# Optimization experiments

Hardware: AMD Instinct MI355X
Metric: run time of the kernel (lower is better)

## Reference

```python
import jax, jax.numpy as jnp
import numpy as np

B, T, C = 4, 2048, 1024
N_HEAD = 16
HEAD_DIM = C // N_HEAD


def setup_inputs() -> dict:
    key = jax.random.key(0)
    k1, k2, k3, k4, k5 = jax.random.split(key, 5)
    s = 0.02
    return {
        "x": jax.random.normal(k1, (B, T, C), dtype=jnp.float32),
        "w_attn": jax.random.normal(k2, (C, 3 * C), dtype=jnp.float32) * s,
        "b_attn": jnp.zeros((3 * C,), dtype=jnp.float32),
        "w_proj": jax.random.normal(k3, (C, C), dtype=jnp.float32) * s,
        "b_proj": jnp.zeros((C,), dtype=jnp.float32),
    }


def reference(x, w_attn, b_attn, w_proj, b_proj):
    Bb, Tt, Cc = x.shape
    qkv = x @ w_attn + b_attn                      # [B,T,3C]
    q, k, v = jnp.split(qkv, 3, axis=-1)
    # [B,T,C] -> [B,H,T,D]
    def heads(t):
        return t.reshape(Bb, Tt, N_HEAD, HEAD_DIM).transpose(0, 2, 1, 3)
    q, k, v = heads(q), heads(k), heads(v)
    scale = 1.0 / (HEAD_DIM ** 0.5)
    att = jnp.einsum('bhqd,bhkd->bhqk', q, k) * scale
    causal = jnp.tril(jnp.ones((Tt, Tt), dtype=bool))
    att = jnp.where(causal, att, -jnp.inf)
    att = jax.nn.softmax(att, axis=-1)             # dropout p=0.0 -> identity
    y = jnp.einsum('bhqk,bhkd->bhqd', att, v)
    y = y.transpose(0, 2, 1, 3).reshape(Bb, Tt, Cc)
    return y @ w_proj + b_proj
```

## Files before the change

kernel.cpp:

```cpp
#include <hip/hip_runtime.h>
#include <hip/hip_bf16.h>

typedef unsigned short u16;
typedef unsigned int u32;
typedef __bf16 bf16_t;
typedef bf16_t bf16x8 __attribute__((ext_vector_type(8)));
typedef float f32x4 __attribute__((ext_vector_type(4)));
typedef u16 u16x4 __attribute__((ext_vector_type(4)));
typedef u32 u32x2 __attribute__((ext_vector_type(2)));
typedef u32 u32x4 __attribute__((ext_vector_type(4)));
typedef int intx2 __attribute__((ext_vector_type(2)));

#define MFMA16(a, b, c) __builtin_amdgcn_mfma_f32_16x16x32_bf16((a), (b), (c), 0, 0, 0)

#define QSCL 0.18033688011112042f

__device__ __forceinline__ u16 f2b(float f) {
  bf16_t h = (bf16_t)f;
  return __builtin_bit_cast(u16, h);
}

__device__ __forceinline__ void gload_lds16(const void* src, void* dst) {
  __builtin_amdgcn_global_load_lds(
      (const __attribute__((address_space(1))) void*)src,
      (__attribute__((address_space(3))) void*)dst, 16, 0, 0);
}

__device__ __forceinline__ bf16x8 frag_read(const u16* tile, int row, int kchunk) {
  int off = row * 128 + ((kchunk ^ (row & 7)) << 4);
  return *reinterpret_cast<const bf16x8*>(reinterpret_cast<const char*>(tile) + off);
}

__device__ __forceinline__ void stage128(const u16* g, int rowStrideElts, u16* tile, int tid) {
  int lane = tid & 63, w = tid >> 6;
#pragma unroll
  for (int i = 0; i < 4; ++i) {
    int r = w * 32 + i * 8 + (lane >> 3);
    int cs = (lane & 7) ^ (r & 7);
    gload_lds16(g + (size_t)r * rowStrideElts + cs * 8, tile + r * 64 + (lane & 7) * 8);
  }
}

__global__ __launch_bounds__(256) void cvt_f32_bf16(const float* __restrict__ in,
                                                    u16* __restrict__ out, int n4) {
  int i = blockIdx.x * 256 + threadIdx.x;
  if (i < n4) {
    float4 f = reinterpret_cast<const float4*>(in)[i];
    ushort4 o;
    o.x = f2b(f.x); o.y = f2b(f.y); o.z = f2b(f.z); o.w = f2b(f.w);
    reinterpret_cast<ushort4*>(out)[i] = o;
  }
}

__global__ __launch_bounds__(256) void transpose_cvt(const float* __restrict__ in,
                                                     u16* __restrict__ out, int K, int N) {
  __shared__ float t[32][33];
  int n0 = blockIdx.x * 32, k0 = blockIdx.y * 32;
  int tx = threadIdx.x & 31, ty = threadIdx.x >> 5;
#pragma unroll
  for (int i = 0; i < 32; i += 8)
    t[ty + i][tx] = in[(size_t)(k0 + ty + i) * N + n0 + tx];
  __syncthreads();
#pragma unroll
  for (int i = 0; i < 32; i += 8)
    out[(size_t)(n0 + ty + i) * K + k0 + tx] = f2b(t[tx][ty + i]);
}

__global__ __launch_bounds__(256) void gemm_qkv(const u16* __restrict__ xb,
                                                const u16* __restrict__ waT,
                                                const float* __restrict__ bias,
                                                u16* __restrict__ q, u16* __restrict__ kk,
                                                u16* __restrict__ vt) {
  __shared__ u16 lA[128 * 64];
  __shared__ u16 lB[128 * 64];
  int tid = threadIdx.x, lane = tid & 63, w = tid >> 6;
  int wr = w >> 1, wc = w & 1;
  int bm = blockIdx.x, bn = blockIdx.y;
  f32x4 acc[4][4] = {};
  const u16* gA = xb + (size_t)bm * 128 * 1024;
  const u16* gB = waT + (size_t)bn * 128 * 1024;
  for (int k0 = 0; k0 < 1024; k0 += 64) {
    stage128(gA + k0, 1024, lA, tid);
    stage128(gB + k0, 1024, lB, tid);
    __syncthreads();
#pragma unroll
    for (int s = 0; s < 2; ++s) {
      bf16x8 af[4], bfr[4];
#pragma unroll
      for (int mi = 0; mi < 4; ++mi)
        af[mi] = frag_read(lA, wr * 64 + mi * 16 + (lane & 15), (lane >> 4) + s * 4);
#pragma unroll
      for (int ni = 0; ni < 4; ++ni)
        bfr[ni] = frag_read(lB, wc * 64 + ni * 16 + (lane & 15), (lane >> 4) + s * 4);
#pragma unroll
      for (int mi = 0; mi < 4; ++mi)
#pragma unroll
        for (int ni = 0; ni < 4; ++ni)
          acc[mi][ni] = MFMA16(af[mi], bfr[ni], acc[mi][ni]);
    }
    __syncthreads();
  }
  int m0 = bm * 128 + wr * 64;
  int n0 = bn * 128 + wc * 64;
#pragma unroll
  for (int ni = 0; ni < 4; ++ni) {
    int col = n0 + ni * 16 + (lane & 15);
    float bv = bias[col];
    int part = col >> 10;
    int cin = col & 1023;
    int h = cin >> 6, d = cin & 63;
    float fct = (part == 0) ? QSCL : 1.0f;
#pragma unroll
    for (int mi = 0; mi < 4; ++mi) {
#pragma unroll
      for (int j = 0; j < 4; ++j) {
        int row = m0 + mi * 16 + (lane >> 4) * 4 + j;
        int b = row >> 11, t = row & 2047;
        u16 hv = f2b((acc[mi][ni][j] + bv) * fct);
        if (part == 0)
          q[(((size_t)(b * 16 + h) * 2048 + t) << 6) + d] = hv;
        else if (part == 1)
          kk[(((size_t)(b * 16 + h) * 2048 + t) << 6) + d] = hv;
        else
          vt[(((size_t)(b * 16 + h) << 6) + d) * 2048 + t] = hv;
      }
    }
  }
}

__global__ __launch_bounds__(256) void gemm_proj(const u16* __restrict__ att,
                                                 const u16* __restrict__ wpT,
                                                 const float* __restrict__ bias,
                                                 float* __restrict__ out) {
  __shared__ u16 lA[128 * 64];
  __shared__ u16 lB[128 * 64];
  int tid = threadIdx.x, lane = tid & 63, w = tid >> 6;
  int wr = w >> 1, wc = w & 1;
  int bm = blockIdx.x, bn = blockIdx.y;
  f32x4 acc[4][4] = {};
  const u16* gA = att + (size_t)bm * 128 * 1024;
  const u16* gB = wpT + (size_t)bn * 128 * 1024;
  for (int k0 = 0; k0 < 1024; k0 += 64) {
    stage128(gA + k0, 1024, lA, tid);
    stage128(gB + k0, 1024, lB, tid);
    __syncthreads();
#pragma unroll
    for (int s = 0; s < 2; ++s) {
      bf16x8 af[4], bfr[4];
#pragma unroll
      for (int mi = 0; mi < 4; ++mi)
        af[mi] = frag_read(lA, wr * 64 + mi * 16 + (lane & 15), (lane >> 4) + s * 4);
#pragma unroll
      for (int ni = 0; ni < 4; ++ni)
        bfr[ni] = frag_read(lB, wc * 64 + ni * 16 + (lane & 15), (lane >> 4) + s * 4);
#pragma unroll
      for (int mi = 0; mi < 4; ++mi)
#pragma unroll
        for (int ni = 0; ni < 4; ++ni)
          acc[mi][ni] = MFMA16(af[mi], bfr[ni], acc[mi][ni]);
    }
    __syncthreads();
  }
  int m0 = bm * 128 + wr * 64;
  int n0 = bn * 128 + wc * 64;
#pragma unroll
  for (int ni = 0; ni < 4; ++ni) {
    int col = n0 + ni * 16 + (lane & 15);
    float bv = bias[col];
#pragma unroll
    for (int mi = 0; mi < 4; ++mi)
#pragma unroll
      for (int j = 0; j < 4; ++j) {
        int row = m0 + mi * 16 + (lane >> 4) * 4 + j;
        out[(size_t)row * 1024 + col] = acc[mi][ni][j] + bv;
      }
  }
}


__device__ __forceinline__ void stage_kv(const u16* kb, const u16* vb, int kt,
                                         u16* lK, u16* lV, int tid) {
  int lane = tid & 63, w = tid >> 6;
#pragma unroll
  for (int i = 0; i < 2; ++i) {
    int r = w * 16 + i * 8 + (lane >> 3);
    int cs = (lane & 7) ^ (r & 7);
    gload_lds16(kb + (size_t)(kt * 64 + r) * 64 + cs * 8, lK + r * 64 + (lane & 7) * 8);
    gload_lds16(vb + (size_t)r * 2048 + kt * 64 + cs * 8, lV + r * 64 + (lane & 7) * 8);
  }
}

__device__ __forceinline__ bf16x8 pdist(u32 a0, u32 a1, u32 b0, u32 b1, bool odd) {
  intx2 r0 = __builtin_amdgcn_permlane32_swap((int)a0, (int)b0, false, false);
  intx2 r1 = __builtin_amdgcn_permlane32_swap((int)a1, (int)b1, false, false);
  u32 x0 = __shfl_xor((u32)r0[1], 16, 64);
  u32 x1 = __shfl_xor((u32)r1[1], 16, 64);
  u32 y0 = __shfl_xor((u32)r0[0], 16, 64);
  u32 y1 = __shfl_xor((u32)r1[0], 16, 64);
  u32x4 f;
  f[0] = odd ? x0 : (u32)r0[0];
  f[1] = odd ? x1 : (u32)r1[0];
  f[2] = odd ? (u32)r0[1] : y0;
  f[3] = odd ? (u32)r1[1] : y1;
  return __builtin_bit_cast(bf16x8, f);
}

__global__ __launch_bounds__(256, 4) void attn_fwd(const u16* __restrict__ q,
                                                   const u16* __restrict__ kk,
                                                   const u16* __restrict__ vt,
                                                   u16* __restrict__ att) {
  __shared__ u16 lK[2][64 * 64];
  __shared__ u16 lV[2][64 * 64];
  int tid = threadIdx.x, lane = tid & 63, w = tid >> 6;
  int ln = lane & 15, g = lane >> 4;
  int gh = g >> 1, gl = g & 1;
  bool godd = (g & 1) != 0;
  int bh = blockIdx.x;
  int qtA = blockIdx.y;
  int qtB = 31 - qtA;
  const u16* qb = q + (size_t)bh * 2048 * 64;
  const u16* kb = kk + (size_t)bh * 2048 * 64;
  const u16* vb = vt + (size_t)bh * 64 * 2048;
  int q0A = qtA * 64 + w * 16;
  int q0B = qtB * 64 + w * 16;

  bf16x8 aqA[2], aqB[2];
  {
    const u16* pa = qb + (size_t)(q0A + ln) * 64 + g * 8;
    const u16* pb = qb + (size_t)(q0B + ln) * 64 + g * 8;
    aqA[0] = *reinterpret_cast<const bf16x8*>(pa);
    aqA[1] = *reinterpret_cast<const bf16x8*>(pa + 32);
    aqB[0] = *reinterpret_cast<const bf16x8*>(pb);
    aqB[1] = *reinterpret_cast<const bf16x8*>(pb + 32);
  }

  float mA = -1e30f, lA = 0.f, mB = -1e30f, lB = 0.f;
  f32x4 oA[4] = {}, oB[4] = {};

  auto softmax_state = [&](f32x4* sf, float& m_r, float& l_r, f32x4* o,
                           bool domask, int k0, int qg,
                           bf16x8& pf0, bf16x8& pf1) {
    if (domask) {
#pragma unroll
      for (int kc = 0; kc < 4; ++kc)
#pragma unroll
        for (int j = 0; j < 4; ++j)
          if (k0 + kc * 16 + g * 4 + j > qg) sf[kc][j] = -1e30f;
    }
    f32x4 m4;
#pragma unroll
    for (int j = 0; j < 4; ++j)
      m4[j] = fmaxf(fmaxf(sf[0][j], sf[1][j]), fmaxf(sf[2][j], sf[3][j]));
    float mxl = fmaxf(fmaxf(m4[0], m4[1]), fmaxf(m4[2], m4[3]));
    if (!__all(mxl - m_r <= 8.f)) {
      float mx = fmaxf(mxl, __shfl_xor(mxl, 16, 64));
      mx = fmaxf(mx, __shfl_xor(mx, 32, 64));
      mx = fmaxf(m_r, mx);
      float sc = __builtin_amdgcn_exp2f(m_r - mx);
      m_r = mx;
      l_r *= sc;
#pragma unroll
      for (int dc = 0; dc < 4; ++dc) o[dc] *= sc;
    }
    u32 d0[4], d1[4];
    float rs = 0.f;
#pragma unroll
    for (int kc = 0; kc < 4; ++kc) {
      u16x4 v4;
#pragma unroll
      for (int j = 0; j < 4; ++j) {
        float p = __builtin_amdgcn_exp2f(sf[kc][j] - m_r);
        rs += p;
        v4[j] = f2b(p);
      }
      u32x2 dd = __builtin_bit_cast(u32x2, v4);
      d0[kc] = dd[0];
      d1[kc] = dd[1];
    }
    l_r += rs;
    pf0 = pdist(d0[0], d1[0], d0[1], d1[1], godd);
    pf1 = pdist(d0[2], d1[2], d0[3], d1[3], godd);
  };

  stage_kv(kb, vb, 0, &lK[0][0], &lV[0][0], tid);

  for (int kt = 0; kt <= qtB; ++kt) {
    int cur = kt & 1;
    __syncthreads();
    if (kt < qtB) stage_kv(kb, vb, kt + 1, &lK[cur ^ 1][0], &lV[cur ^ 1][0], tid);
    const u16* Kt = &lK[cur][0];
    const u16* Vt = &lV[cur][0];
    bool doA = (kt <= qtA);

    f32x4 sB[4], sA[4];
    __builtin_amdgcn_s_setprio(1);
#pragma unroll
    for (int kc = 0; kc < 4; ++kc) {
      f32x4 zB = {}, zA = {};
#pragma unroll
      for (int s = 0; s < 2; ++s) {
        bf16x8 kf = frag_read(Kt, kc * 16 + ln, g + 4 * s);
        zB = MFMA16(kf, aqB[s], zB);
        if (doA) zA = MFMA16(kf, aqA[s], zA);
      }
      sB[kc] = zB;
      sA[kc] = zA;
    }
    __builtin_amdgcn_s_setprio(0);

    bf16x8 pB0, pB1, pA0, pA1;
    softmax_state(sB, mB, lB, oB, kt == qtB, kt * 64, q0B + ln, pB0, pB1);
    if (doA) softmax_state(sA, mA, lA, oA, kt == qtA, kt * 64, q0A + ln, pA0, pA1);

    __builtin_amdgcn_s_setprio(1);
#pragma unroll
    for (int dc = 0; dc < 4; ++dc) {
      bf16x8 v0 = frag_read(Vt, dc * 16 + ln, g);
      bf16x8 v1 = frag_read(Vt, dc * 16 + ln, g + 4);
      oB[dc] = MFMA16(v0, pB0, oB[dc]);
      oB[dc] = MFMA16(v1, pB1, oB[dc]);
      if (doA) {
        oA[dc] = MFMA16(v0, pA0, oA[dc]);
        oA[dc] = MFMA16(v1, pA1, oA[dc]);
      }
    }
    __builtin_amdgcn_s_setprio(0);
  }

  __syncthreads();
  u16* lPw = &lK[0][0] + w * 1024;
  int prow = ln * 128;
  int xorq = (ln & 7) << 4;
  int b = bh >> 4, h = bh & 15;
  auto epi = [&](const f32x4* o, float l_r, int q0w) {
    float lt = l_r + __shfl_xor(l_r, 16, 64);
    lt += __shfl_xor(lt, 32, 64);
    float inv = __builtin_amdgcn_rcpf(lt);
#pragma unroll
    for (int dc = 0; dc < 4; ++dc) {
      u16x4 v4;
#pragma unroll
      for (int j = 0; j < 4; ++j) v4[j] = f2b(o[dc][j] * inv);
      *reinterpret_cast<u16x4*>(reinterpret_cast<char*>(lPw) + prow +
                                ((((dc << 1) + gh) << 4) ^ xorq) + gl * 8) = v4;
    }
    asm volatile("s_waitcnt lgkmcnt(0)" ::: "memory");
    __builtin_amdgcn_sched_barrier(0);
    __builtin_amdgcn_wave_barrier();
    bf16x8 r0 = frag_read(lPw, ln, g);
    bf16x8 r1 = frag_read(lPw, ln, g + 4);
    __builtin_amdgcn_sched_barrier(0);
    int t = q0w + ln;
    u16* dst = att + (size_t)(b * 2048 + t) * 1024 + h * 64;
    *reinterpret_cast<bf16x8*>(dst + g * 8) = r0;
    *reinterpret_cast<bf16x8*>(dst + 32 + g * 8) = r1;
  };
  epi(oB, lB, q0B);
  epi(oA, lA, q0A);
}

extern "C" void kernel_launch(void* const* d_in, const int* in_sizes, int n_in,
                              void* d_out, int out_size, void* d_ws, size_t ws_size,
                              hipStream_t stream) {
  const float* x = (const float*)d_in[0];
  const float* w_attn = (const float*)d_in[1];
  const float* b_attn = (const float*)d_in[2];
  const float* w_proj = (const float*)d_in[3];
  const float* b_proj = (const float*)d_in[4];
  float* out = (float*)d_out;

  u16* ws = (u16*)d_ws;
  u16* xb = ws;
  u16* waT = xb + 8388608;
  u16* wpT = waT + 3145728;
  u16* vtx = wpT + 1048576;
  u16* att = xb;
  u16* qx = (u16*)d_out;
  u16* kx = qx + 8388608;

  cvt_f32_bf16<<<8192, 256, 0, stream>>>(x, xb, 2097152);
  transpose_cvt<<<dim3(96, 32), 256, 0, stream>>>(w_attn, waT, 1024, 3072);
  transpose_cvt<<<dim3(32, 32), 256, 0, stream>>>(w_proj, wpT, 1024, 1024);
  gemm_qkv<<<dim3(64, 24), 256, 0, stream>>>(xb, waT, b_attn, qx, kx, vtx);
  attn_fwd<<<dim3(64, 16), 256, 0, stream>>>(qx, kx, vtx, att);
  gemm_proj<<<dim3(64, 8), 256, 0, stream>>>(att, wpT, b_proj, out);
}
```

Baseline: 209.1 us.

## Triple-buffer K/V staging with prefetch depth two and interleave softmax with PV MFMAs

Moves the K/V LDS staging from double to triple buffering. Loads run two tiles ahead, gated by explicit vmcnt waits and a raw s_barrier instead of __syncthreads. V fragments are hoisted into registers before softmax, and the B-tile PV MFMAs are placed before the A-tile softmax so matrix work can overlap the exponent math. This costs 50% more LDS, more registers, and a lower occupancy hint (3 blocks instead of 4). The hand-written vmcnt(4) count relies on stage_kv issuing exactly that many loads.

```diff
diff --git a/kernel.cpp b/kernel.cpp
--- a/kernel.cpp
+++ b/kernel.cpp
@@ -205,12 +205,12 @@
   return __builtin_bit_cast(bf16x8, f);
 }
 
-__global__ __launch_bounds__(256, 4) void attn_fwd(const u16* __restrict__ q,
+__global__ __launch_bounds__(256, 3) void attn_fwd(const u16* __restrict__ q,
                                                    const u16* __restrict__ kk,
                                                    const u16* __restrict__ vt,
                                                    u16* __restrict__ att) {
-  __shared__ u16 lK[2][64 * 64];
-  __shared__ u16 lV[2][64 * 64];
+  __shared__ u16 lK[3][64 * 64];
+  __shared__ u16 lV[3][64 * 64];
   int tid = threadIdx.x, lane = tid & 63, w = tid >> 6;
   int ln = lane & 15, g = lane >> 4;
   int gh = g >> 1, gl = g & 1;
@@ -283,11 +283,21 @@
   };
 
   stage_kv(kb, vb, 0, &lK[0][0], &lV[0][0], tid);
+  stage_kv(kb, vb, 1, &lK[1][0], &lV[1][0], tid);
 
   for (int kt = 0; kt <= qtB; ++kt) {
-    int cur = kt & 1;
-    __syncthreads();
-    if (kt < qtB) stage_kv(kb, vb, kt + 1, &lK[cur ^ 1][0], &lV[cur ^ 1][0], tid);
+    if (kt < qtB) {
+      asm volatile("s_waitcnt vmcnt(4)" ::: "memory");
+    } else {
+      asm volatile("s_waitcnt vmcnt(0)" ::: "memory");
+    }
+    __builtin_amdgcn_s_barrier();
+    if (kt + 2 <= qtB) {
+      int nb = kt + 2 - ((kt + 2) >= 3 ? 3 : 0);
+      nb = (kt + 2) % 3;
+      stage_kv(kb, vb, kt + 2, &lK[nb][0], &lV[nb][0], tid);
+    }
+    int cur = kt % 3;
     const u16* Kt = &lK[cur][0];
     const u16* Vt = &lV[cur][0];
     bool doA = (kt <= qtA);
@@ -308,23 +318,32 @@
     }
     __builtin_amdgcn_s_setprio(0);
 
+    bf16x8 vf0[4], vf1[4];
+#pragma unroll
+    for (int dc = 0; dc < 4; ++dc) {
+      vf0[dc] = frag_read(Vt, dc * 16 + ln, g);
+      vf1[dc] = frag_read(Vt, dc * 16 + ln, g + 4);
+    }
+
     bf16x8 pB0, pB1, pA0, pA1;
     softmax_state(sB, mB, lB, oB, kt == qtB, kt * 64, q0B + ln, pB0, pB1);
-    if (doA) softmax_state(sA, mA, lA, oA, kt == qtA, kt * 64, q0A + ln, pA0, pA1);
-
     __builtin_amdgcn_s_setprio(1);
 #pragma unroll
     for (int dc = 0; dc < 4; ++dc) {
-      bf16x8 v0 = frag_read(Vt, dc * 16 + ln, g);
-      bf16x8 v1 = frag_read(Vt, dc * 16 + ln, g + 4);
-      oB[dc] = MFMA16(v0, pB0, oB[dc]);
-      oB[dc] = MFMA16(v1, pB1, oB[dc]);
-      if (doA) {
-        oA[dc] = MFMA16(v0, pA0, oA[dc]);
-        oA[dc] = MFMA16(v1, pA1, oA[dc]);
+      oB[dc] = MFMA16(vf0[dc], pB0, oB[dc]);
+      oB[dc] = MFMA16(vf1[dc], pB1, oB[dc]);
+    }
+    __builtin_amdgcn_s_setprio(0);
+    if (doA) {
+      softmax_state(sA, mA, lA, oA, kt == qtA, kt * 64, q0A + ln, pA0, pA1);
+      __builtin_amdgcn_s_setprio(1);
+#pragma unroll
+      for (int dc = 0; dc < 4; ++dc) {
+        oA[dc] = MFMA16(vf0[dc], pA0, oA[dc]);
+        oA[dc] = MFMA16(vf1[dc], pA1, oA[dc]);
       }
-    }
-    __builtin_amdgcn_s_setprio(0);
+      __builtin_amdgcn_s_setprio(0);
+    }
   }
 
   __syncthreads();
```

New measurement: 203.4 us. 2.7% less time.
